# Kernel tuning notes

Measured on AMD Instinct MI355X. Metric: run time of the kernel, lower is better.

The kernel has to match this reference:

```python
import jax, jax.numpy as jnp
import numpy as np


def setup_inputs() -> dict:
    key = jax.random.key(0)
    k_x, k_g, k_fc, k_pj = jax.random.split(key, 4)
    B, T, C, H, E = 4, 2048, 1024, 2048, 8
    n_layer = 12
    x = jax.random.normal(k_x, (B, T, C), dtype=jnp.float32)
    w_gate = 0.02 * jax.random.normal(k_g, (C, E), dtype=jnp.float32)
    w_fc = 0.02 * jax.random.normal(k_fc, (C, H, E), dtype=jnp.float32)
    w_proj = (0.02 * (2 * n_layer) ** -0.5) * jax.random.normal(k_pj, (H, C, E), dtype=jnp.float32)
    return {"x": x, "w_gate": w_gate, "w_fc": w_fc, "w_proj": w_proj, "top_k": 2}


def reference(x, w_gate, w_fc, w_proj, top_k):
    # x: (B,T,C); w_gate: (C,E); w_fc: (C,H,E); w_proj: (H,C,E)
    E = w_gate.shape[-1]
    gate = jnp.einsum('btc,ce->bte', x, w_gate)                  # gating logits
    top_vals, top_idx = jax.lax.top_k(gate, top_k)               # (B,T,K) — raw logits used as combine weights (as in source)
    # Per-expert combine weight: sum_k top_val_k * onehot(idx_k) — zero for unselected experts.
    # This is mathematically identical to gathering the K expert weight slices per token
    # (the source's gather+einsum) but avoids the (B,T,C,H,K) weight blowup.
    onehot = jax.nn.one_hot(top_idx, E, dtype=x.dtype)           # (B,T,K,E)
    w_e = jnp.einsum('btk,btke->bte', top_vals, onehot)          # (B,T,E)
    h = jax.nn.silu(jnp.einsum('btc,che->bthe', x, w_fc))        # (B,T,H,E)
    o = jnp.einsum('bthe,bte,hce->btc', h, w_e, w_proj)          # weighted expert combine
    return o
```

## Files before the change

kernel.cpp:

```cpp
#include <hip/hip_runtime.h>
#include <hip/hip_bf16.h>


#define NTOK 8192
#define CD   1024
#define HD   2048
#define NE   8
#define NSLOT 16384
#define MTILES 20
#define BK   64

typedef short  short4_t  __attribute__((ext_vector_type(4)));
typedef short  short8_t  __attribute__((ext_vector_type(8)));
typedef __bf16 bf16x8_t  __attribute__((ext_vector_type(8)));
typedef float  f32x4_t   __attribute__((ext_vector_type(4)));

struct FragArg {
  short8_t v;
  __device__ operator short8_t() const { return v; }
  __device__ operator bf16x8_t() const { return __builtin_bit_cast(bf16x8_t, v); }
};

static __device__ __forceinline__ float b2f(unsigned short u) {
  union { float f; unsigned int i; } w; w.i = ((unsigned int)u) << 16; return w.f;
}
static __device__ __forceinline__ unsigned short f2b(float f) {
  unsigned int u = __float_as_uint(f);
  u += 0x7fffu + ((u >> 16) & 1u);
  return (unsigned short)(u >> 16);
}
static __device__ __forceinline__ void gl2lds16(const void* g, void* l) {
  __builtin_amdgcn_global_load_lds((__attribute__((address_space(1))) void*)g,
                                   (__attribute__((address_space(3))) void*)l,
                                   16, 0, 0);
}

#define GATE_BLOCKS (NTOK / 4)
__global__ __launch_bounds__(256) void prep_kernel(
    const float* __restrict__ x, const float* __restrict__ wg,
    const float* __restrict__ wfc, const float* __restrict__ wpj,
    unsigned short* __restrict__ xb,
    unsigned short* __restrict__ wfcp, unsigned short* __restrict__ wpjp,
    int* __restrict__ tok_e, float* __restrict__ tok_v,
    int* __restrict__ g_counts)
{
  __shared__ __align__(16) unsigned short lds[NE * 32 * 40];
  __shared__ int hist[NE];
  int t = threadIdx.x;

  if (blockIdx.x < GATE_BLOCKS) {
    if (t < NE) hist[t] = 0;
    __syncthreads();
    int wv = t >> 6, lane = t & 63;
    int tk = blockIdx.x * 4 + wv;
    const float* xr = x + (size_t)tk * CD;
    unsigned short* xbr = xb + (size_t)tk * CD;
    float acc[NE] = {0, 0, 0, 0, 0, 0, 0, 0};
    #pragma unroll
    for (int jj = 0; jj < 4; ++jj) {
      int c0 = (lane + 64 * jj) * 4;
      float4 xv = *(const float4*)(xr + c0);
      short4_t ob;
      ob[0] = (short)f2b(xv.x); ob[1] = (short)f2b(xv.y);
      ob[2] = (short)f2b(xv.z); ob[3] = (short)f2b(xv.w);
      *(short4_t*)(xbr + c0) = ob;
      #pragma unroll
      for (int j = 0; j < 4; ++j) {
        float xf = (j == 0) ? xv.x : (j == 1) ? xv.y : (j == 2) ? xv.z : xv.w;
        const float* wr = wg + (size_t)(c0 + j) * NE;
        float4 w0 = *(const float4*)wr;
        float4 w1 = *(const float4*)(wr + 4);
        acc[0] += xf * w0.x; acc[1] += xf * w0.y;
        acc[2] += xf * w0.z; acc[3] += xf * w0.w;
        acc[4] += xf * w1.x; acc[5] += xf * w1.y;
        acc[6] += xf * w1.z; acc[7] += xf * w1.w;
      }
    }
    #pragma unroll
    for (int off = 32; off >= 1; off >>= 1)
      #pragma unroll
      for (int e = 0; e < NE; ++e) acc[e] += __shfl_down(acc[e], off, 64);
    if (lane == 0) {
      float v1 = -3.0e38f, v2 = -3.0e38f; int i1 = 0, i2 = 1;
      #pragma unroll
      for (int e = 0; e < NE; ++e) {
        float g = acc[e];
        if (g > v1) { v2 = v1; i2 = i1; v1 = g; i1 = e; }
        else if (g > v2) { v2 = g; i2 = e; }
      }
      tok_e[tk * 2] = i1; tok_e[tk * 2 + 1] = i2;
      tok_v[tk * 2] = v1; tok_v[tk * 2 + 1] = v2;
      atomicAdd(&hist[i1], 1); atomicAdd(&hist[i2], 1);
    }
    __syncthreads();
    if (t < NE && hist[t] > 0) atomicAdd(&g_counts[t], hist[t]);
  } else {
    int pid = blockIdx.x - GATE_BLOCKS;
    int tensor = pid >> 11;
    int rem = pid & 2047;
    int bx = rem & 63, by = rem >> 6;
    const float* in; unsigned short* out; int D0, D1, b0, b1;
    if (tensor == 0) { in = wfc; out = wfcp; D0 = CD; D1 = HD;
                       b1 = bx * 32; b0 = by * 32; }
    else             { in = wpj; out = wpjp; D0 = HD; D1 = CD;
                       b1 = by * 32; b0 = bx * 32; }
    int d1i = t & 31, d0q = t >> 5;
    #pragma unroll
    for (int r = 0; r < 4; ++r) {
      int d0i = d0q * 4 + r;
      const float* src = in + ((size_t)(b0 + d0i) * D1 + (b1 + d1i)) * NE;
      float4 v0 = *(const float4*)src;
      float4 v1 = *(const float4*)(src + 4);
      unsigned short* dst0 = &lds[d1i * 40 + d0i];
      dst0[0 * 32 * 40] = f2b(v0.x);
      dst0[1 * 32 * 40] = f2b(v0.y);
      dst0[2 * 32 * 40] = f2b(v0.z);
      dst0[3 * 32 * 40] = f2b(v0.w);
      dst0[4 * 32 * 40] = f2b(v1.x);
      dst0[5 * 32 * 40] = f2b(v1.y);
      dst0[6 * 32 * 40] = f2b(v1.z);
      dst0[7 * 32 * 40] = f2b(v1.w);
    }
    __syncthreads();
    int dchunk = t & 3, d1w = (t >> 2) & 31, ehalf = t >> 7;
    #pragma unroll
    for (int p = 0; p < 4; ++p) {
      int e = ehalf + 2 * p;
      short8_t v = *(const short8_t*)&lds[e * 32 * 40 + d1w * 40 + dchunk * 8];
      *(short8_t*)(out + ((size_t)e * D1 + (b1 + d1w)) * D0 + b0 + dchunk * 8) = v;
    }
  }
}

__global__ __launch_bounds__(256) void scatter_kernel(
    const int* __restrict__ tok_e, const float* __restrict__ tok_v,
    const int* __restrict__ g_counts, int* __restrict__ g_cursor,
    int* __restrict__ g_base,
    int* __restrict__ bucket_tok, float* __restrict__ bucket_v,
    int* __restrict__ slot_of)
{
  int gid = blockIdx.x * 256 + threadIdx.x;
  int lane = threadIdx.x & 63;
  int base[NE];
  { int o = 0;
    #pragma unroll
    for (int e = 0; e < NE; ++e) { base[e] = o; o += g_counts[e]; } }
  int e = tok_e[gid];
  unsigned long long lanebit = 1ull << lane;
  int pos = 0;
  #pragma unroll
  for (int ee = 0; ee < NE; ++ee) {
    unsigned long long m = __ballot(e == ee);
    if (e == ee) {
      int leader = __ffsll((long long)m) - 1;
      int cnt = __popcll(m);
      int start = 0;
      if (lane == leader) start = atomicAdd(&g_cursor[ee], cnt);
      start = __shfl(start, leader, 64);
      pos = start + __popcll(m & (lanebit - 1));
    }
  }
  int sl = base[e] + pos;
  bucket_tok[sl] = gid >> 1;
  bucket_v[sl]   = tok_v[gid];
  slot_of[gid]   = sl;
  if (gid < NE) g_base[gid] = base[gid];
}

__global__ __launch_bounds__(256) void gemm1_kernel(
    const unsigned short* __restrict__ xb, const unsigned short* __restrict__ wfcp,
    const int* __restrict__ g_counts, const int* __restrict__ g_base,
    const int* __restrict__ bucket_tok, const float* __restrict__ bucket_v,
    unsigned short* __restrict__ hbuf)
{
  int id = blockIdx.x;
  int e = id & 7;
  int r = id >> 3;
  int nt = r & 15;
  int mt = r >> 4;

  int cnt = g_counts[e];
  int m0 = mt * 128;
  if (m0 >= cnt) return;
  int base = g_base[e];
  int n0 = nt * 128;

  __shared__ __align__(16) unsigned short lsA[128 * BK];
  __shared__ __align__(16) unsigned short lsB[128 * BK];
  __shared__ int   s_tok[128];
  __shared__ float s_v[128];

  int t = threadIdx.x;
  if (t < 128) {
    int ok = (m0 + t) < cnt;
    s_tok[t] = ok ? bucket_tok[base + m0 + t] : 0;
    s_v[t]   = ok ? bucket_v[base + m0 + t] : 0.0f;
  }
  __syncthreads();

  int lane = t & 63, wv = t >> 6;
  int subrow = lane >> 3, kc = lane & 7;
  const unsigned short* pA[4]; const unsigned short* pB[4];
  unsigned short* dA[4]; unsigned short* dB[4];
  #pragma unroll
  for (int p = 0; p < 4; ++p) {
    int rr = p * 32 + wv * 8 + subrow;
    int gc = kc ^ ((rr >> 1) & 7);
    pA[p] = xb + (size_t)s_tok[rr] * CD + gc * 8;
    pB[p] = wfcp + ((size_t)e * HD + n0 + rr) * CD + gc * 8;
    dA[p] = &lsA[(p * 32 + wv * 8) * BK];
    dB[p] = &lsB[(p * 32 + wv * 8) * BK];
  }

  int wm = (wv & 1) * 64, wn = (wv >> 1) * 64;
  int ml = lane & 15, kq = lane >> 4;

  f32x4_t acc[4][4];
  #pragma unroll
  for (int i = 0; i < 4; ++i)
    #pragma unroll
    for (int j = 0; j < 4; ++j) acc[i][j] = (f32x4_t){0.f, 0.f, 0.f, 0.f};

  for (int k0 = 0; k0 < CD; k0 += BK) {
    __syncthreads();
    #pragma unroll
    for (int p = 0; p < 4; ++p) {
      gl2lds16(pA[p], dA[p]); pA[p] += BK;
      gl2lds16(pB[p], dB[p]); pB[p] += BK;
    }
    __syncthreads();
    #pragma unroll
    for (int s = 0; s < 2; ++s) {
      short8_t af[4], bfr[4];
      #pragma unroll
      for (int i = 0; i < 4; ++i) {
        int ar = wm + i * 16 + ml;
        af[i]  = *(const short8_t*)&lsA[ar * BK + (((s * 4 + kq) ^ ((ar >> 1) & 7)) * 8)];
        int br = wn + i * 16 + ml;
        bfr[i] = *(const short8_t*)&lsB[br * BK + (((s * 4 + kq) ^ ((br >> 1) & 7)) * 8)];
      }
      #pragma unroll
      for (int i = 0; i < 4; ++i)
        #pragma unroll
        for (int j = 0; j < 4; ++j)
          acc[i][j] = __builtin_amdgcn_mfma_f32_16x16x32_bf16(
              FragArg{af[i]}, FragArg{bfr[j]}, acc[i][j], 0, 0, 0);
    }
  }

  #pragma unroll
  for (int i = 0; i < 4; ++i) {
    int rb = wm + i * 16 + kq * 4;
    #pragma unroll
    for (int r2 = 0; r2 < 4; ++r2) {
      int row = rb + r2;
      if (m0 + row < cnt) {
        float v = s_v[row];
        size_t ro = (size_t)(base + m0 + row) * HD + n0;
        #pragma unroll
        for (int j = 0; j < 4; ++j) {
          float z = acc[i][j][r2];
          float val = v * (z / (1.0f + __expf(-z)));
          hbuf[ro + wn + j * 16 + ml] = f2b(val);
        }
      }
    }
  }
}

__global__ __launch_bounds__(256) void gemm2_kernel(
    const unsigned short* __restrict__ hbuf, const unsigned short* __restrict__ wpjp,
    const int* __restrict__ g_counts, const int* __restrict__ g_base,
    unsigned short* __restrict__ oslot)
{
  int id = blockIdx.x;
  int e = id & 7;
  int r = id >> 3;
  int nt = r & 7;
  int mt = r >> 3;

  int cnt = g_counts[e];
  int m0 = mt * 128;
  if (m0 >= cnt) return;
  int base = g_base[e];
  int n0 = nt * 128;

  __shared__ __align__(16) unsigned short lsA[128 * BK];
  __shared__ __align__(16) unsigned short lsB[128 * BK];

  int t = threadIdx.x;
  int lane = t & 63, wv = t >> 6;
  int subrow = lane >> 3, kc = lane & 7;
  const unsigned short* pA[4]; const unsigned short* pB[4];
  unsigned short* dA[4]; unsigned short* dB[4];
  #pragma unroll
  for (int p = 0; p < 4; ++p) {
    int rr = p * 32 + wv * 8 + subrow;
    int gc = kc ^ ((rr >> 1) & 7);
    pA[p] = hbuf + ((size_t)(base + m0 + rr)) * HD + gc * 8;
    pB[p] = wpjp + ((size_t)e * CD + n0 + rr) * HD + gc * 8;
    dA[p] = &lsA[(p * 32 + wv * 8) * BK];
    dB[p] = &lsB[(p * 32 + wv * 8) * BK];
  }

  int wm = (wv & 1) * 64, wn = (wv >> 1) * 64;
  int ml = lane & 15, kq = lane >> 4;

  f32x4_t acc[4][4];
  #pragma unroll
  for (int i = 0; i < 4; ++i)
    #pragma unroll
    for (int j = 0; j < 4; ++j) acc[i][j] = (f32x4_t){0.f, 0.f, 0.f, 0.f};

  for (int k0 = 0; k0 < HD; k0 += BK) {
    __syncthreads();
    #pragma unroll
    for (int p = 0; p < 4; ++p) {
      gl2lds16(pA[p], dA[p]); pA[p] += BK;
      gl2lds16(pB[p], dB[p]); pB[p] += BK;
    }
    __syncthreads();
    #pragma unroll
    for (int s = 0; s < 2; ++s) {
      short8_t af[4], bfr[4];
      #pragma unroll
      for (int i = 0; i < 4; ++i) {
        int ar = wm + i * 16 + ml;
        af[i]  = *(const short8_t*)&lsA[ar * BK + (((s * 4 + kq) ^ ((ar >> 1) & 7)) * 8)];
        int br = wn + i * 16 + ml;
        bfr[i] = *(const short8_t*)&lsB[br * BK + (((s * 4 + kq) ^ ((br >> 1) & 7)) * 8)];
      }
      #pragma unroll
      for (int i = 0; i < 4; ++i)
        #pragma unroll
        for (int j = 0; j < 4; ++j)
          acc[i][j] = __builtin_amdgcn_mfma_f32_16x16x32_bf16(
              FragArg{af[i]}, FragArg{bfr[j]}, acc[i][j], 0, 0, 0);
    }
  }

  #pragma unroll
  for (int i = 0; i < 4; ++i) {
    int rb = wm + i * 16 + kq * 4;
    #pragma unroll
    for (int r2 = 0; r2 < 4; ++r2) {
      int row = rb + r2;
      if (m0 + row < cnt) {
        size_t ro = (size_t)(base + m0 + row) * CD + n0;
        #pragma unroll
        for (int j = 0; j < 4; ++j)
          oslot[ro + wn + j * 16 + ml] = f2b(acc[i][j][r2]);
      }
    }
  }
}

__global__ __launch_bounds__(256) void combine_kernel(
    const unsigned short* __restrict__ oslot, const int* __restrict__ slot_of,
    float* __restrict__ out)
{
  int gid = blockIdx.x * 256 + threadIdx.x;
  int tk = gid >> 7;
  int ch = (gid & 127) * 8;
  int s0 = slot_of[tk * 2], s1 = slot_of[tk * 2 + 1];
  short8_t a = *(const short8_t*)(oslot + (size_t)s0 * CD + ch);
  short8_t b = *(const short8_t*)(oslot + (size_t)s1 * CD + ch);
  float* op = out + (size_t)tk * CD + ch;
  float4 o0, o1;
  o0.x = b2f((unsigned short)a[0]) + b2f((unsigned short)b[0]);
  o0.y = b2f((unsigned short)a[1]) + b2f((unsigned short)b[1]);
  o0.z = b2f((unsigned short)a[2]) + b2f((unsigned short)b[2]);
  o0.w = b2f((unsigned short)a[3]) + b2f((unsigned short)b[3]);
  o1.x = b2f((unsigned short)a[4]) + b2f((unsigned short)b[4]);
  o1.y = b2f((unsigned short)a[5]) + b2f((unsigned short)b[5]);
  o1.z = b2f((unsigned short)a[6]) + b2f((unsigned short)b[6]);
  o1.w = b2f((unsigned short)a[7]) + b2f((unsigned short)b[7]);
  *(float4*)op = o0;
  *(float4*)(op + 4) = o1;
}

extern "C" void kernel_launch(void* const* d_in, const int* in_sizes, int n_in,
                              void* d_out, int out_size, void* d_ws, size_t ws_size,
                              hipStream_t stream)
{
  const float* x   = (const float*)d_in[0];
  const float* wg  = (const float*)d_in[1];
  const float* wfc = (const float*)d_in[2];
  const float* wpj = (const float*)d_in[3];
  float* out = (float*)d_out;

  char* w = (char*)d_ws;
  unsigned short* wfcp  = (unsigned short*)w; w += (size_t)NE * HD * CD * 2;
  unsigned short* wpjp  = (unsigned short*)w; w += (size_t)NE * CD * HD * 2;
  unsigned short* xb    = (unsigned short*)w; w += (size_t)NTOK * CD * 2;
  unsigned short* hbuf  = (unsigned short*)w; w += (size_t)NSLOT * HD * 2;
  unsigned short* oslot = (unsigned short*)w; w += (size_t)NSLOT * CD * 2;
  int*   tok_e      = (int*)w;   w += NSLOT * 4;
  float* tok_v      = (float*)w; w += NSLOT * 4;
  int*   slot_of    = (int*)w;   w += NSLOT * 4;
  int*   bucket_tok = (int*)w;   w += NSLOT * 4;
  float* bucket_v   = (float*)w; w += NSLOT * 4;
  int*   g_counts   = (int*)w;   w += NE * 4;
  int*   g_cursor   = (int*)w;   w += NE * 4;
  int*   g_base     = (int*)w;   w += 256;

  hipMemsetAsync(g_counts, 0, 2 * NE * sizeof(int), stream);
  prep_kernel<<<GATE_BLOCKS + 4096, 256, 0, stream>>>(
      x, wg, wfc, wpj, xb, wfcp, wpjp, tok_e, tok_v, g_counts);
  scatter_kernel<<<NSLOT / 256, 256, 0, stream>>>(
      tok_e, tok_v, g_counts, g_cursor, g_base, bucket_tok, bucket_v, slot_of);
  gemm1_kernel<<<(HD / 128) * MTILES * NE, 256, 0, stream>>>(
      xb, wfcp, g_counts, g_base, bucket_tok, bucket_v, hbuf);
  gemm2_kernel<<<(CD / 128) * MTILES * NE, 256, 0, stream>>>(
      hbuf, wpjp, g_counts, g_base, oslot);
  combine_kernel<<<(NTOK * CD / 8) / 256, 256, 0, stream>>>(oslot, slot_of, out);
}
```

Measured before the change: 454.3 us.

## Move w_proj packing from prep kernel into gemm1 launch to overlap

The fp32-to-bf16 transpose-pack of w_proj moves out of prep_kernel and into extra leading blocks of gemm1_kernel, which gemm2 consumes afterwards. The pack code is factored into a shared helper, and gemm1's LDS buffers are merged into one array that the pack blocks reuse. The aim is to shorten the serial prep phase and let the memory-bound packing overlap with the compute-bound expert GEMM. In exchange, gemm1 launches more blocks, and pack blocks scheduled first may delay GEMM tiles or compete with them for bandwidth.

```diff
diff --git a/kernel.cpp b/kernel.cpp
--- a/kernel.cpp
+++ b/kernel.cpp
@@ -9,6 +9,7 @@
 #define NSLOT 16384
 #define MTILES 20
 #define BK   64
+#define PACK_BLOCKS 2048
 
 typedef short  short4_t  __attribute__((ext_vector_type(4)));
 typedef short  short8_t  __attribute__((ext_vector_type(8)));
@@ -35,12 +36,42 @@
                                    16, 0, 0);
 }
 
+static __device__ __forceinline__ void pack_tile(
+    const float* __restrict__ in, unsigned short* __restrict__ out,
+    int D0, int D1, int b0, int b1, unsigned short* smem, int t)
+{
+  int d1i = t & 31, d0q = t >> 5;
+  #pragma unroll
+  for (int r = 0; r < 4; ++r) {
+    int d0i = d0q * 4 + r;
+    const float* src = in + ((size_t)(b0 + d0i) * D1 + (b1 + d1i)) * NE;
+    float4 v0 = *(const float4*)src;
+    float4 v1 = *(const float4*)(src + 4);
+    unsigned short* dst0 = &smem[d1i * 40 + d0i];
+    dst0[0 * 32 * 40] = f2b(v0.x);
+    dst0[1 * 32 * 40] = f2b(v0.y);
+    dst0[2 * 32 * 40] = f2b(v0.z);
+    dst0[3 * 32 * 40] = f2b(v0.w);
+    dst0[4 * 32 * 40] = f2b(v1.x);
+    dst0[5 * 32 * 40] = f2b(v1.y);
+    dst0[6 * 32 * 40] = f2b(v1.z);
+    dst0[7 * 32 * 40] = f2b(v1.w);
+  }
+  __syncthreads();
+  int dchunk = t & 3, d1w = (t >> 2) & 31, ehalf = t >> 7;
+  #pragma unroll
+  for (int p = 0; p < 4; ++p) {
+    int e = ehalf + 2 * p;
+    short8_t v = *(const short8_t*)&smem[e * 32 * 40 + d1w * 40 + dchunk * 8];
+    *(short8_t*)(out + ((size_t)e * D1 + (b1 + d1w)) * D0 + b0 + dchunk * 8) = v;
+  }
+}
+
 #define GATE_BLOCKS (NTOK / 4)
 __global__ __launch_bounds__(256) void prep_kernel(
     const float* __restrict__ x, const float* __restrict__ wg,
-    const float* __restrict__ wfc, const float* __restrict__ wpj,
-    unsigned short* __restrict__ xb,
-    unsigned short* __restrict__ wfcp, unsigned short* __restrict__ wpjp,
+    const float* __restrict__ wfc,
+    unsigned short* __restrict__ xb, unsigned short* __restrict__ wfcp,
     int* __restrict__ tok_e, float* __restrict__ tok_v,
     int* __restrict__ g_counts)
 {
@@ -96,39 +127,8 @@
     if (t < NE && hist[t] > 0) atomicAdd(&g_counts[t], hist[t]);
   } else {
     int pid = blockIdx.x - GATE_BLOCKS;
-    int tensor = pid >> 11;
-    int rem = pid & 2047;
-    int bx = rem & 63, by = rem >> 6;
-    const float* in; unsigned short* out; int D0, D1, b0, b1;
-    if (tensor == 0) { in = wfc; out = wfcp; D0 = CD; D1 = HD;
-                       b1 = bx * 32; b0 = by * 32; }
-    else             { in = wpj; out = wpjp; D0 = HD; D1 = CD;
-                       b1 = by * 32; b0 = bx * 32; }
-    int d1i = t & 31, d0q = t >> 5;
-    #pragma unroll
-    for (int r = 0; r < 4; ++r) {
-      int d0i = d0q * 4 + r;
-      const float* src = in + ((size_t)(b0 + d0i) * D1 + (b1 + d1i)) * NE;
-      float4 v0 = *(const float4*)src;
-      float4 v1 = *(const float4*)(src + 4);
-      unsigned short* dst0 = &lds[d1i * 40 + d0i];
-      dst0[0 * 32 * 40] = f2b(v0.x);
-      dst0[1 * 32 * 40] = f2b(v0.y);
-      dst0[2 * 32 * 40] = f2b(v0.z);
-      dst0[3 * 32 * 40] = f2b(v0.w);
-      dst0[4 * 32 * 40] = f2b(v1.x);
-      dst0[5 * 32 * 40] = f2b(v1.y);
-      dst0[6 * 32 * 40] = f2b(v1.z);
-      dst0[7 * 32 * 40] = f2b(v1.w);
-    }
-    __syncthreads();
-    int dchunk = t & 3, d1w = (t >> 2) & 31, ehalf = t >> 7;
-    #pragma unroll
-    for (int p = 0; p < 4; ++p) {
-      int e = ehalf + 2 * p;
-      short8_t v = *(const short8_t*)&lds[e * 32 * 40 + d1w * 40 + dchunk * 8];
-      *(short8_t*)(out + ((size_t)e * D1 + (b1 + d1w)) * D0 + b0 + dchunk * 8) = v;
-    }
+    int bx = pid & 63, by = pid >> 6;
+    pack_tile(wfc, wfcp, CD, HD, by * 32, bx * 32, lds, t);
   }
 }
 
@@ -169,11 +169,24 @@
 
 __global__ __launch_bounds__(256) void gemm1_kernel(
     const unsigned short* __restrict__ xb, const unsigned short* __restrict__ wfcp,
+    const float* __restrict__ wpj, unsigned short* __restrict__ wpjp,
     const int* __restrict__ g_counts, const int* __restrict__ g_base,
     const int* __restrict__ bucket_tok, const float* __restrict__ bucket_v,
     unsigned short* __restrict__ hbuf)
 {
-  int id = blockIdx.x;
+  __shared__ __align__(16) unsigned short smem[128 * BK * 2];
+  __shared__ int   s_tok[128];
+  __shared__ float s_v[128];
+  int t = threadIdx.x;
+
+  if (blockIdx.x < PACK_BLOCKS) {
+    int pid = blockIdx.x;
+    int bx = pid & 63, by = pid >> 6;
+    pack_tile(wpj, wpjp, HD, CD, bx * 32, by * 32, smem, t);
+    return;
+  }
+
+  int id = blockIdx.x - PACK_BLOCKS;
   int e = id & 7;
   int r = id >> 3;
   int nt = r & 15;
@@ -185,12 +198,9 @@
   int base = g_base[e];
   int n0 = nt * 128;
 
-  __shared__ __align__(16) unsigned short lsA[128 * BK];
-  __shared__ __align__(16) unsigned short lsB[128 * BK];
-  __shared__ int   s_tok[128];
-  __shared__ float s_v[128];
-
-  int t = threadIdx.x;
+  unsigned short* lsA = smem;
+  unsigned short* lsB = smem + 128 * BK;
+
   if (t < 128) {
     int ok = (m0 + t) < cnt;
     s_tok[t] = ok ? bucket_tok[base + m0 + t] : 0;
@@ -405,12 +415,12 @@
   int*   g_base     = (int*)w;   w += 256;
 
   hipMemsetAsync(g_counts, 0, 2 * NE * sizeof(int), stream);
-  prep_kernel<<<GATE_BLOCKS + 4096, 256, 0, stream>>>(
-      x, wg, wfc, wpj, xb, wfcp, wpjp, tok_e, tok_v, g_counts);
+  prep_kernel<<<GATE_BLOCKS + PACK_BLOCKS, 256, 0, stream>>>(
+      x, wg, wfc, xb, wfcp, tok_e, tok_v, g_counts);
   scatter_kernel<<<NSLOT / 256, 256, 0, stream>>>(
       tok_e, tok_v, g_counts, g_cursor, g_base, bucket_tok, bucket_v, slot_of);
-  gemm1_kernel<<<(HD / 128) * MTILES * NE, 256, 0, stream>>>(
-      xb, wfcp, g_counts, g_base, bucket_tok, bucket_v, hbuf);
+  gemm1_kernel<<<PACK_BLOCKS + (HD / 128) * MTILES * NE, 256, 0, stream>>>(
+      xb, wfcp, wpj, wpjp, g_counts, g_base, bucket_tok, bucket_v, hbuf);
   gemm2_kernel<<<(CD / 128) * MTILES * NE, 256, 0, stream>>>(
       hbuf, wpjp, g_counts, g_base, oslot);
   combine_kernel<<<(NTOK * CD / 8) / 256, 256, 0, stream>>>(oslot, slot_of, out);
```

Measured after the change: 451.9 us. About the same (-0.5%).
